# Performance work log

Hardware: AMD Instinct MI355X
Metric: run time of the kernel (lower is better)

The kernel has to match this reference:

```python
import jax, jax.numpy as jnp
import numpy as np

EMBED_DIM = 768
NUM_HEADS = 12
HEAD_DIM = EMBED_DIM // NUM_HEADS
MEMORY_SIZE = 64
B, T = 8, 1024


def setup_inputs() -> dict:
    key = jax.random.key(0)
    ks = jax.random.split(key, 8)
    s = 0.02
    return {
        "x": jax.random.normal(ks[0], (B, T, EMBED_DIM), dtype=jnp.float32),
        "w_qkv": jax.random.normal(ks[1], (EMBED_DIM, 3 * EMBED_DIM), dtype=jnp.float32) * s,
        "b_qkv": jax.random.normal(ks[2], (3 * EMBED_DIM,), dtype=jnp.float32) * s,
        "w_out": jax.random.normal(ks[3], (EMBED_DIM, EMBED_DIM), dtype=jnp.float32) * s,
        "b_out": jax.random.normal(ks[4], (EMBED_DIM,), dtype=jnp.float32) * s,
        "w_mem": jax.random.normal(ks[5], (EMBED_DIM, EMBED_DIM), dtype=jnp.float32) * s,
        "b_mem": jax.random.normal(ks[6], (EMBED_DIM,), dtype=jnp.float32) * s,
        "memory": jax.random.normal(ks[7], (1, MEMORY_SIZE, EMBED_DIM), dtype=jnp.float32),
    }


def reference(x, w_qkv, b_qkv, w_out, b_out, w_mem, b_mem, memory):
    Bx, Tx, C = x.shape
    H, D = NUM_HEADS, HEAD_DIM
    scale = 1.0 / np.sqrt(D).astype(np.float32)

    # qkv projection -> (3, B, H, T, D)
    qkv = (x @ w_qkv + b_qkv).reshape(Bx, Tx, 3, H, D)
    qkv = jnp.transpose(qkv, (2, 0, 3, 1, 4))
    q, k, v = qkv[0], qkv[1], qkv[2]

    # full (non-causal) local attention over T
    scores = jnp.einsum("bhqd,bhkd->bhqk", q, k) * scale  # (B,H,T,T)
    local_out = jnp.einsum("bhqk,bhkd->bhqd", jax.nn.softmax(scores, axis=-1), v)

    # memory attention: projected memory serves as both K and V
    mem = memory @ w_mem + b_mem                      # (1, M, C)
    mem = jnp.broadcast_to(mem, (Bx, MEMORY_SIZE, C))
    mem_kv = jnp.transpose(mem.reshape(Bx, MEMORY_SIZE, H, D), (0, 2, 1, 3))  # (B,H,M,D)
    mem_scores = jnp.einsum("bhqd,bhmd->bhqm", q, mem_kv) * scale
    mem_out = jnp.einsum("bhqm,bhmd->bhqd", jax.nn.softmax(mem_scores, axis=-1), mem_kv)

    out = (local_out + mem_out).transpose(0, 2, 1, 3).reshape(Bx, Tx, C)
    return out @ w_out + b_out
```

## Files before the change

### kernel.cpp

```cpp
#include <hip/hip_runtime.h>

#define EMBED 768
#define NH 12
#define HD 64
#define MEMN 64
#define BB 8
#define TT 1024
#define ROWS 8192
#define QKV_N 2304
#define QSZ 6291456

typedef short bf16x8_t __attribute__((ext_vector_type(8)));
typedef float f32x4_t __attribute__((ext_vector_type(4)));

__device__ __forceinline__ unsigned short f2b(float f){
    union { float f; unsigned int i; } v; v.f = f;
    unsigned int x = v.i;
    unsigned int r = x + 0x7fffu + ((x >> 16) & 1u);
    return (unsigned short)(r >> 16);
}
__device__ __forceinline__ unsigned short f2b_ru(float f){
    union { float f; unsigned int i; } v; v.f = f;
    return (unsigned short)((v.i + 0x8000u) >> 16);
}

__device__ __forceinline__ void gl16(const unsigned short* g, unsigned short* l){
    __builtin_amdgcn_global_load_lds(
        (const __attribute__((address_space(1))) void*)g,
        (__attribute__((address_space(3))) void*)l,
        16, 0, 0);
}

#define PREP_CVT   3072
#define PREP_TQKV  4800
#define PREP_TOUT  5376
#define PREP_TOTAL 5388

__global__ __launch_bounds__(256) void prep_kernel(
    const float* __restrict__ x,
    const float* __restrict__ w_qkv,
    const float* __restrict__ w_out,
    const float* __restrict__ memory,
    const float* __restrict__ w_mem,
    const float* __restrict__ b_mem,
    unsigned short* __restrict__ xb,
    unsigned short* __restrict__ wqkvT,
    unsigned short* __restrict__ woutT,
    unsigned short* __restrict__ mem_k,
    unsigned short* __restrict__ mem_v)
{
    __shared__ unsigned short pool[5120];
    const int bid = blockIdx.x;
    const int t = threadIdx.x;

    if (bid < PREP_CVT) {
        int i = bid * 2048 + t * 8;
        float4 f0 = *(const float4*)&x[i];
        float4 f1 = *(const float4*)&x[i + 4];
        union { bf16x8_t v; unsigned short s[8]; } u;
        u.s[0] = f2b(f0.x); u.s[1] = f2b(f0.y); u.s[2] = f2b(f0.z); u.s[3] = f2b(f0.w);
        u.s[4] = f2b(f1.x); u.s[5] = f2b(f1.y); u.s[6] = f2b(f1.z); u.s[7] = f2b(f1.w);
        *(bf16x8_t*)&xb[i] = u.v;
    } else if (bid < PREP_TOUT) {
        const float* in; unsigned short* out; int R, C, loc;
        if (bid < PREP_TQKV) { in = w_qkv; out = wqkvT; R = EMBED; C = QKV_N; loc = bid - PREP_CVT; }
        else                 { in = w_out; out = woutT; R = EMBED; C = EMBED; loc = bid - PREP_TQKV; }
        int nbc = C / 32;
        int bc = (loc % nbc) * 32, br = (loc / nbc) * 32;
        unsigned short (*tile)[33] = (unsigned short(*)[33])pool;
        int lr = t >> 5, lc = t & 31;
        for (int i = 0; i < 4; i++) {
            int r = lr + i * 8;
            tile[r][lc] = f2b(in[(size_t)(br + r) * C + bc + lc]);
        }
        __syncthreads();
        for (int i = 0; i < 4; i++) {
            int r = lr + i * 8;
            out[(size_t)(bc + r) * R + br + lc] = tile[lc][r];
        }
    } else {
        unsigned short (*As)[40] = (unsigned short(*)[40])pool;
        unsigned short (*Bs)[40] = (unsigned short(*)[40])(pool + 2560);
        int wave = t >> 6, lane = t & 63;
        int ln = lane & 15, lq = lane >> 4;
        int bn = (bid - PREP_TOUT) * 64;
        const int K = EMBED, N = EMBED;

        f32x4_t acc[4];
        for (int i = 0; i < 4; i++) acc[i] = (f32x4_t)(0.f);
        int sm = t >> 2, sk = (t & 3) * 8;
        int bk = t >> 3, bn8 = (t & 7) * 8;

        for (int k0 = 0; k0 < K; k0 += 32) {
            __syncthreads();
            {
                float4 f0 = *(const float4*)&memory[(size_t)sm * K + k0 + sk];
                float4 f1 = *(const float4*)&memory[(size_t)sm * K + k0 + sk + 4];
                unsigned short* ap = &As[sm][sk];
                ap[0] = f2b(f0.x); ap[1] = f2b(f0.y); ap[2] = f2b(f0.z); ap[3] = f2b(f0.w);
                ap[4] = f2b(f1.x); ap[5] = f2b(f1.y); ap[6] = f2b(f1.z); ap[7] = f2b(f1.w);
            }
            {
                float4 g0 = *(const float4*)&w_mem[(size_t)(k0 + bk) * N + bn + bn8];
                float4 g1 = *(const float4*)&w_mem[(size_t)(k0 + bk) * N + bn + bn8 + 4];
                Bs[bn8 + 0][bk] = f2b(g0.x); Bs[bn8 + 1][bk] = f2b(g0.y);
                Bs[bn8 + 2][bk] = f2b(g0.z); Bs[bn8 + 3][bk] = f2b(g0.w);
                Bs[bn8 + 4][bk] = f2b(g1.x); Bs[bn8 + 5][bk] = f2b(g1.y);
                Bs[bn8 + 6][bk] = f2b(g1.z); Bs[bn8 + 7][bk] = f2b(g1.w);
            }
            __syncthreads();
            bf16x8_t a = *(bf16x8_t*)&As[wave * 16 + ln][lq * 8];
            for (int nt = 0; nt < 4; nt++) {
                bf16x8_t bf = *(bf16x8_t*)&Bs[nt * 16 + ln][lq * 8];
                acc[nt] = __builtin_amdgcn_mfma_f32_16x16x32_bf16(a, bf, acc[nt], 0, 0, 0);
            }
        }
        for (int nt = 0; nt < 4; nt++) {
            int c = bn + nt * 16 + ln;
            float bv = b_mem[c];
            for (int r = 0; r < 4; r++) {
                int row = wave * 16 + lq * 4 + r;
                int h = c >> 6, d = c & 63;
                unsigned short o = f2b(acc[nt][r] + bv);
                mem_k[((h * 64 + row) << 6) + d] = o;
                mem_v[((h * 64 + d) << 6) + row] = o;
            }
        }
    }
}

__global__ __launch_bounds__(256) void vtrans_kernel(
    const unsigned short* __restrict__ in, unsigned short* __restrict__ out)
{
    __shared__ unsigned short tile[64][72];
    int t0 = blockIdx.x * 64;
    int bh = blockIdx.y;
    const unsigned short* ip = in + ((size_t)bh * TT + t0) * 64;
    unsigned short* op = out + ((size_t)bh * 64) * TT + t0;
    int t = threadIdx.x;
    for (int i = 0; i < 2; i++) {
        int idx = i * 256 + t;
        int r = idx >> 3, c8 = (idx & 7) * 8;
        *(bf16x8_t*)&tile[r][c8] = *(const bf16x8_t*)&ip[(size_t)r * 64 + c8];
    }
    __syncthreads();
    for (int i = 0; i < 2; i++) {
        int idx = i * 256 + t;
        int d = idx >> 3, tc8 = (idx & 7) * 8;
        union { bf16x8_t v; unsigned short s[8]; } u;
        for (int j = 0; j < 8; j++) u.s[j] = tile[tc8 + j][d];
        *(bf16x8_t*)&op[(size_t)d * TT + tc8] = u.v;
    }
}

__global__ __launch_bounds__(512) void gemm512(
    const unsigned short* __restrict__ A,
    const unsigned short* __restrict__ BT,
    const float* __restrict__ bias,
    unsigned short* __restrict__ dq,
    unsigned short* __restrict__ dkv,
    int M, int N, int K)
{
    __shared__ unsigned short As[16384];
    __shared__ unsigned short Bs[8192];
    const int t = threadIdx.x;
    const int wave = t >> 6, lane = t & 63;
    const int ln = lane & 15, lq = lane >> 4;
    const int wm = (wave >> 1) * 64, wn = (wave & 1) * 64;
    const int bm = blockIdx.y * 256, bn = blockIdx.x * 128;

    f32x4_t acc[4][4];
    for (int i = 0; i < 4; i++)
        for (int j = 0; j < 4; j++) acc[i][j] = (f32x4_t)(0.f);

    const int rl8 = lane >> 3;
    const int swz = ((lane & 7) ^ rl8) * 8;
    const unsigned short* Ap = A + (size_t)(bm + wave * 32 + rl8) * K + swz;
    const unsigned short* Bp = BT + (size_t)(bn + wave * 16 + rl8) * K + swz;
    unsigned short* asd = &As[wave * 2048];
    unsigned short* bsd = &Bs[wave * 1024];

    const int e0 = (lq ^ (ln & 7)) * 8;
    const int e1 = e0 ^ 32;

    for (int k0 = 0; k0 < K; k0 += 64) {
        __syncthreads();
        for (int i = 0; i < 4; i++)
            gl16(Ap + (size_t)(i * 8) * K + k0, asd + i * 512);
        for (int i = 0; i < 2; i++)
            gl16(Bp + (size_t)(i * 8) * K + k0, bsd + i * 512);
        __syncthreads();

        {
            bf16x8_t af[4], bfr[4];
            for (int mt = 0; mt < 4; mt++)
                af[mt] = *(bf16x8_t*)&As[(wm + mt * 16 + ln) * 64 + e0];
            for (int nt = 0; nt < 4; nt++)
                bfr[nt] = *(bf16x8_t*)&Bs[(wn + nt * 16 + ln) * 64 + e0];
            for (int mt = 0; mt < 4; mt++)
                for (int nt = 0; nt < 4; nt++)
                    acc[mt][nt] = __builtin_amdgcn_mfma_f32_16x16x32_bf16(
                        af[mt], bfr[nt], acc[mt][nt], 0, 0, 0);
        }
        {
            bf16x8_t af[4], bfr[4];
            for (int mt = 0; mt < 4; mt++)
                af[mt] = *(bf16x8_t*)&As[(wm + mt * 16 + ln) * 64 + e1];
            for (int nt = 0; nt < 4; nt++)
                bfr[nt] = *(bf16x8_t*)&Bs[(wn + nt * 16 + ln) * 64 + e1];
            for (int mt = 0; mt < 4; mt++)
                for (int nt = 0; nt < 4; nt++)
                    acc[mt][nt] = __builtin_amdgcn_mfma_f32_16x16x32_bf16(
                        af[mt], bfr[nt], acc[mt][nt], 0, 0, 0);
        }
    }

    const float QSCALE = 0.125f * 1.44269504088896340736f;
    const int s = bn / 768;
    for (int nt = 0; nt < 4; nt++) {
        int c = bn + wn + nt * 16 + ln;
        int rem = c - s * 768;
        int h = rem >> 6, d = rem & 63;
        float bv = bias[c];
        for (int mt = 0; mt < 4; mt++) {
            for (int r = 0; r < 4; r++) {
                int row = bm + wm + mt * 16 + lq * 4 + r;
                float val = acc[mt][nt][r] + bv;
                if (s == 0) {
                    dq[(size_t)row * 768 + rem] = f2b(val * QSCALE);
                } else {
                    int bb = row >> 10, tt = row & 1023;
                    dkv[(size_t)(s - 1) * QSZ +
                        (((size_t)(bb * 12 + h) * 1024 + tt) << 6) + d] = f2b(val);
                }
            }
        }
    }
}

__global__ __launch_bounds__(256) void gemm_bt(
    const unsigned short* __restrict__ A,
    const unsigned short* __restrict__ BT,
    const float* __restrict__ bias,
    float* __restrict__ df,
    int M, int N, int K)
{
    __shared__ unsigned short As[8192];
    __shared__ unsigned short Bs[8192];
    const int t = threadIdx.x;
    const int wave = t >> 6, lane = t & 63;
    const int ln = lane & 15, lq = lane >> 4;
    const int wm = (wave >> 1) * 64, wn = (wave & 1) * 64;
    const int bm = blockIdx.y * 128, bn = blockIdx.x * 128;

    f32x4_t acc[4][4];
    for (int i = 0; i < 4; i++)
        for (int j = 0; j < 4; j++) acc[i][j] = (f32x4_t)(0.f);

    const int rl8 = lane >> 3;
    const int swz = ((lane & 7) ^ rl8) * 8;
    const unsigned short* Ap = A + (size_t)(bm + wave * 32 + rl8) * K + swz;
    const unsigned short* Bp = BT + (size_t)(bn + wave * 32 + rl8) * K + swz;
    unsigned short* asd = &As[wave * 2048];
    unsigned short* bsd = &Bs[wave * 2048];

    const int e0 = (lq ^ (ln & 7)) * 8;
    const int e1 = e0 ^ 32;

    for (int k0 = 0; k0 < K; k0 += 64) {
        __syncthreads();
        for (int i = 0; i < 4; i++) {
            gl16(Ap + (size_t)(i * 8) * K + k0, asd + i * 512);
            gl16(Bp + (size_t)(i * 8) * K + k0, bsd + i * 512);
        }
        __syncthreads();

        {
            bf16x8_t af[4], bfr[4];
            for (int mt = 0; mt < 4; mt++)
                af[mt] = *(bf16x8_t*)&As[(wm + mt * 16 + ln) * 64 + e0];
            for (int nt = 0; nt < 4; nt++)
                bfr[nt] = *(bf16x8_t*)&Bs[(wn + nt * 16 + ln) * 64 + e0];
            for (int mt = 0; mt < 4; mt++)
                for (int nt = 0; nt < 4; nt++)
                    acc[mt][nt] = __builtin_amdgcn_mfma_f32_16x16x32_bf16(
                        af[mt], bfr[nt], acc[mt][nt], 0, 0, 0);
        }
        {
            bf16x8_t af[4], bfr[4];
            for (int mt = 0; mt < 4; mt++)
                af[mt] = *(bf16x8_t*)&As[(wm + mt * 16 + ln) * 64 + e1];
            for (int nt = 0; nt < 4; nt++)
                bfr[nt] = *(bf16x8_t*)&Bs[(wn + nt * 16 + ln) * 64 + e1];
            for (int mt = 0; mt < 4; mt++)
                for (int nt = 0; nt < 4; nt++)
                    acc[mt][nt] = __builtin_amdgcn_mfma_f32_16x16x32_bf16(
                        af[mt], bfr[nt], acc[mt][nt], 0, 0, 0);
        }
    }

    for (int nt = 0; nt < 4; nt++) {
        int c = bn + wn + nt * 16 + ln;
        float bv = bias[c];
        for (int mt = 0; mt < 4; mt++)
            for (int r = 0; r < 4; r++) {
                int row = bm + wm + mt * 16 + lq * 4 + r;
                df[(size_t)row * N + c] = acc[mt][nt][r] + bv;
            }
    }
}

__global__ __launch_bounds__(512) void attn_kernel(
    unsigned short* __restrict__ qio,
    const unsigned short* __restrict__ k_ws,
    const unsigned short* __restrict__ vT_ws,
    const unsigned short* __restrict__ mem_k,
    const unsigned short* __restrict__ mem_v)
{
    __shared__ unsigned short Qs[8192];
    __shared__ unsigned short Ks[8192];
    __shared__ unsigned short Vs[8192];
    unsigned short* Ps = Qs;

    const int t = threadIdx.x;
    const int wave = t >> 6, lane = t & 63;
    const int ln = lane & 15, lq = lane >> 4;
    const int rl = lane >> 3;
    const int cl = ((lane & 7) ^ rl) * 8;

    int bid = blockIdx.x;
    int xcd = bid & 7, rest = bid >> 3;
    int bh = xcd * 12 + (rest >> 3);
    int qt = rest & 7;
    int b = bh / 12, h = bh - b * 12;

    unsigned short* qp = qio + ((size_t)(b * TT + qt * 128)) * 768 + h * 64;
    const unsigned short* kp = k_ws + (size_t)bh * TT * 64;
    const unsigned short* vp = vT_ws + ((size_t)bh << 16);
    const unsigned short* mkp = mem_k + h * 4096;
    const unsigned short* mvp = mem_v + h * 4096;

    {
        const unsigned short* qg = qp + (size_t)(wave * 16 + rl) * 768 + cl;
        gl16(qg, &Qs[wave * 1024]);
        gl16(qg + (size_t)8 * 768, &Qs[wave * 1024 + 512]);
    }
    __syncthreads();
    const int e0 = (lq ^ (ln & 7)) * 8;
    const int e1 = ((lq ^ (ln & 7)) ^ 4) * 8;
    bf16x8_t aq0 = *(bf16x8_t*)&Qs[(wave * 16 + ln) * 64 + e0];
    bf16x8_t aq1 = *(bf16x8_t*)&Qs[(wave * 16 + ln) * 64 + e1];

    const unsigned short* kg = kp + (wave * 16 + rl) * 64 + cl;
    const unsigned short* vg = vp + (size_t)((wave & 3) * 16 + rl) * 1024 + (wave >> 2) * 64 + cl;

    const int hi3 = ln >> 3, lo3 = ln & 7;
    const int pm = (lq & 1) << 2;
    const int pw0 = (wave * 16 + lq * 4) * 64 + lo3;

    float lsum[4] = {0.f, 0.f, 0.f, 0.f};
    f32x4_t accO[4];
    for (int nt = 0; nt < 4; nt++) accO[nt] = (f32x4_t)(0.f);

    for (int kt = 0; kt < 8; kt++) {
        __syncthreads();
        gl16(kg + kt * 8192,        &Ks[wave * 1024]);
        gl16(kg + kt * 8192 + 512,  &Ks[wave * 1024 + 512]);
        gl16(vg + kt * 128,                 &Vs[wave * 1024]);
        gl16(vg + (size_t)8 * 1024 + kt * 128, &Vs[wave * 1024 + 512]);
        __syncthreads();

        for (int half = 0; half < 2; half++) {
            const unsigned short* Kh = &Ks[half * 4096];
            const unsigned short* Vh = &Vs[half * 4096];
            f32x4_t s[4];
            for (int nt = 0; nt < 4; nt++) s[nt] = (f32x4_t)(0.f);
            for (int nt = 0; nt < 4; nt++)
                s[nt] = __builtin_amdgcn_mfma_f32_16x16x32_bf16(
                    aq0, *(bf16x8_t*)&Kh[(nt * 16 + ln) * 64 + e0], s[nt], 0, 0, 0);
            for (int nt = 0; nt < 4; nt++)
                s[nt] = __builtin_amdgcn_mfma_f32_16x16x32_bf16(
                    aq1, *(bf16x8_t*)&Kh[(nt * 16 + ln) * 64 + e1], s[nt], 0, 0, 0);

            for (int nt = 0; nt < 4; nt++) {
                for (int r = 0; r < 4; r++) {
                    float p = __builtin_amdgcn_exp2f(s[nt][r]);
                    lsum[r] += p;
                    int chp = (nt * 2 + hi3) ^ pm ^ r;
                    Ps[pw0 + r * 64 + chp * 8] = f2b_ru(p);
                }
            }
            bf16x8_t a0 = *(bf16x8_t*)&Ps[(wave * 16 + ln) * 64 + e0];
            bf16x8_t a1 = *(bf16x8_t*)&Ps[(wave * 16 + ln) * 64 + e1];
            for (int nt = 0; nt < 4; nt++) {
                accO[nt] = __builtin_amdgcn_mfma_f32_16x16x32_bf16(
                    a0, *(bf16x8_t*)&Vh[(nt * 16 + ln) * 64 + e0], accO[nt], 0, 0, 0);
                accO[nt] = __builtin_amdgcn_mfma_f32_16x16x32_bf16(
                    a1, *(bf16x8_t*)&Vh[(nt * 16 + ln) * 64 + e1], accO[nt], 0, 0, 0);
            }
        }
    }

    __syncthreads();
    gl16(mkp + (wave * 8 + rl) * 64 + cl, &Ks[wave * 512]);
    gl16(mvp + (wave * 8 + rl) * 64 + cl, &Vs[wave * 512]);
    __syncthreads();

    f32x4_t s2[4];
    for (int nt = 0; nt < 4; nt++) s2[nt] = (f32x4_t)(0.f);
    for (int nt = 0; nt < 4; nt++)
        s2[nt] = __builtin_amdgcn_mfma_f32_16x16x32_bf16(
            aq0, *(bf16x8_t*)&Ks[(nt * 16 + ln) * 64 + e0], s2[nt], 0, 0, 0);
    for (int nt = 0; nt < 4; nt++)
        s2[nt] = __builtin_amdgcn_mfma_f32_16x16x32_bf16(
            aq1, *(bf16x8_t*)&Ks[(nt * 16 + ln) * 64 + e1], s2[nt], 0, 0, 0);

    float l2[4] = {0.f, 0.f, 0.f, 0.f};
    for (int nt = 0; nt < 4; nt++) {
        for (int r = 0; r < 4; r++) {
            float p = __builtin_amdgcn_exp2f(s2[nt][r]);
            l2[r] += p;
            int chp = (nt * 2 + hi3) ^ pm ^ r;
            Ps[pw0 + r * 64 + chp * 8] = f2b_ru(p);
        }
    }
    f32x4_t accM[4];
    for (int nt = 0; nt < 4; nt++) accM[nt] = (f32x4_t)(0.f);
    {
        bf16x8_t a0 = *(bf16x8_t*)&Ps[(wave * 16 + ln) * 64 + e0];
        bf16x8_t a1 = *(bf16x8_t*)&Ps[(wave * 16 + ln) * 64 + e1];
        for (int nt = 0; nt < 4; nt++) {
            accM[nt] = __builtin_amdgcn_mfma_f32_16x16x32_bf16(
                a0, *(bf16x8_t*)&Vs[(nt * 16 + ln) * 64 + e0], accM[nt], 0, 0, 0);
            accM[nt] = __builtin_amdgcn_mfma_f32_16x16x32_bf16(
                a1, *(bf16x8_t*)&Vs[(nt * 16 + ln) * 64 + e1], accM[nt], 0, 0, 0);
        }
    }

    float inv[4], inv2[4];
    for (int r = 0; r < 4; r++) {
        float a = lsum[r], c = l2[r];
        a += __shfl_xor(a, 1); a += __shfl_xor(a, 2);
        a += __shfl_xor(a, 4); a += __shfl_xor(a, 8);
        c += __shfl_xor(c, 1); c += __shfl_xor(c, 2);
        c += __shfl_xor(c, 4); c += __shfl_xor(c, 8);
        inv[r] = 1.f / a;
        inv2[r] = 1.f / c;
    }

    for (int nt = 0; nt < 4; nt++) {
        for (int r = 0; r < 4; r++) {
            int lrow = wave * 16 + lq * 4 + r;
            int lcol = nt * 16 + ln;
            float val = accO[nt][r] * inv[r] + accM[nt][r] * inv2[r];
            qp[(size_t)lrow * 768 + lcol] = f2b(val);
        }
    }
}

extern "C" void kernel_launch(void* const* d_in, const int* in_sizes, int n_in,
                              void* d_out, int out_size, void* d_ws, size_t ws_size,
                              hipStream_t stream) {
    const float* x      = (const float*)d_in[0];
    const float* w_qkv  = (const float*)d_in[1];
    const float* b_qkv  = (const float*)d_in[2];
    const float* w_out  = (const float*)d_in[3];
    const float* b_out  = (const float*)d_in[4];
    const float* w_mem  = (const float*)d_in[5];
    const float* b_mem  = (const float*)d_in[6];
    const float* memory = (const float*)d_in[7];

    unsigned short* ws = (unsigned short*)d_ws;
    unsigned short* q_ws   = ws;
    unsigned short* k_ws   = ws + (size_t)QSZ;
    unsigned short* woutT  = ws + 3 * (size_t)QSZ;
    unsigned short* mem_k  = woutT + (size_t)EMBED * EMBED;
    unsigned short* mem_v  = mem_k + (size_t)NH * MEMN * HD;

    unsigned short* xb    = (unsigned short*)d_out;
    unsigned short* wqkvT = xb + (size_t)QSZ;
    unsigned short* vT    = (unsigned short*)d_out;

    prep_kernel<<<PREP_TOTAL, 256, 0, stream>>>(
        x, w_qkv, w_out, memory, w_mem, b_mem, xb, wqkvT, woutT, mem_k, mem_v);

    gemm512<<<dim3(QKV_N / 128, ROWS / 256), 512, 0, stream>>>(
        xb, wqkvT, b_qkv, q_ws, k_ws, ROWS, QKV_N, EMBED);

    vtrans_kernel<<<dim3(TT / 64, BB * NH), 256, 0, stream>>>(k_ws + (size_t)QSZ, vT);

    attn_kernel<<<8 * NH * BB, 512, 0, stream>>>(q_ws, k_ws, vT, mem_k, mem_v);

    gemm_bt<<<dim3(EMBED / 128, ROWS / 128), 256, 0, stream>>>(
        q_ws, woutT, b_out, (float*)d_out, ROWS, EMBED, EMBED);
}
```

Measured before the change: 245.0 us.

## Double-buffer LDS in QKV and output GEMMs with block remap and MFMA priority

Both GEMM kernels now keep two LDS buffers, so the global-to-LDS loads for the next K tile are issued before computing on the current tile, removing one barrier per iteration. All LDS fragment reads are hoisted ahead of the MFMA chain, and s_setprio raises wave priority around the MFMAs. The QKV GEMM also remaps block IDs in a strided, XCD-aware order to change which tiles run together. The cost is doubled LDS use (96KB for gemm512), which may lower occupancy, and the hardcoded remap constants (72, 18) only fit the 18x32 grid.

```diff
diff --git a/kernel.cpp b/kernel.cpp
--- a/kernel.cpp
+++ b/kernel.cpp
@@ -161,13 +161,17 @@
     unsigned short* __restrict__ dkv,
     int M, int N, int K)
 {
-    __shared__ unsigned short As[16384];
-    __shared__ unsigned short Bs[8192];
+    __shared__ unsigned short As[2][16384];
+    __shared__ unsigned short Bs[2][8192];
     const int t = threadIdx.x;
     const int wave = t >> 6, lane = t & 63;
     const int ln = lane & 15, lq = lane >> 4;
     const int wm = (wave >> 1) * 64, wn = (wave & 1) * 64;
-    const int bm = blockIdx.y * 256, bn = blockIdx.x * 128;
+
+    int bid0 = blockIdx.y * gridDim.x + blockIdx.x;
+    int bid = (bid0 & 7) * 72 + (bid0 >> 3);
+    int by = bid / 18, bx = bid - by * 18;
+    const int bm = by * 256, bn = bx * 128;
 
     f32x4_t acc[4][4];
     for (int i = 0; i < 4; i++)
@@ -177,43 +181,56 @@
     const int swz = ((lane & 7) ^ rl8) * 8;
     const unsigned short* Ap = A + (size_t)(bm + wave * 32 + rl8) * K + swz;
     const unsigned short* Bp = BT + (size_t)(bn + wave * 16 + rl8) * K + swz;
-    unsigned short* asd = &As[wave * 2048];
-    unsigned short* bsd = &Bs[wave * 1024];
 
     const int e0 = (lq ^ (ln & 7)) * 8;
     const int e1 = e0 ^ 32;
 
-    for (int k0 = 0; k0 < K; k0 += 64) {
+    auto compute = [&](const unsigned short* Ac, const unsigned short* Bc) {
+        bf16x8_t af0[4], af1[4], bf0[4], bf1[4];
+#pragma unroll
+        for (int mt = 0; mt < 4; mt++) {
+            af0[mt] = *(const bf16x8_t*)&Ac[(wm + mt * 16 + ln) * 64 + e0];
+            af1[mt] = *(const bf16x8_t*)&Ac[(wm + mt * 16 + ln) * 64 + e1];
+        }
+#pragma unroll
+        for (int nt = 0; nt < 4; nt++) {
+            bf0[nt] = *(const bf16x8_t*)&Bc[(wn + nt * 16 + ln) * 64 + e0];
+            bf1[nt] = *(const bf16x8_t*)&Bc[(wn + nt * 16 + ln) * 64 + e1];
+        }
+        __builtin_amdgcn_s_setprio(1);
+#pragma unroll
+        for (int mt = 0; mt < 4; mt++)
+#pragma unroll
+            for (int nt = 0; nt < 4; nt++)
+                acc[mt][nt] = __builtin_amdgcn_mfma_f32_16x16x32_bf16(
+                    af0[mt], bf0[nt], acc[mt][nt], 0, 0, 0);
+#pragma unroll
+        for (int mt = 0; mt < 4; mt++)
+#pragma unroll
+            for (int nt = 0; nt < 4; nt++)
+                acc[mt][nt] = __builtin_amdgcn_mfma_f32_16x16x32_bf16(
+                    af1[mt], bf1[nt], acc[mt][nt], 0, 0, 0);
+        __builtin_amdgcn_s_setprio(0);
+    };
+
+    for (int i = 0; i < 4; i++)
+        gl16(Ap + (size_t)(i * 8) * K, &As[0][wave * 2048 + i * 512]);
+    for (int i = 0; i < 2; i++)
+        gl16(Bp + (size_t)(i * 8) * K, &Bs[0][wave * 1024 + i * 512]);
+    __syncthreads();
+
+    int cur = 0;
+    for (int k0 = 0; k0 < K - 64; k0 += 64) {
+        const int nb = cur ^ 1;
+        for (int i = 0; i < 4; i++)
+            gl16(Ap + (size_t)(i * 8) * K + k0 + 64, &As[nb][wave * 2048 + i * 512]);
+        for (int i = 0; i < 2; i++)
+            gl16(Bp + (size_t)(i * 8) * K + k0 + 64, &Bs[nb][wave * 1024 + i * 512]);
+        compute(As[cur], Bs[cur]);
         __syncthreads();
-        for (int i = 0; i < 4; i++)
-            gl16(Ap + (size_t)(i * 8) * K + k0, asd + i * 512);
-        for (int i = 0; i < 2; i++)
-            gl16(Bp + (size_t)(i * 8) * K + k0, bsd + i * 512);
-        __syncthreads();
-
-        {
-            bf16x8_t af[4], bfr[4];
-            for (int mt = 0; mt < 4; mt++)
-                af[mt] = *(bf16x8_t*)&As[(wm + mt * 16 + ln) * 64 + e0];
-            for (int nt = 0; nt < 4; nt++)
-                bfr[nt] = *(bf16x8_t*)&Bs[(wn + nt * 16 + ln) * 64 + e0];
-            for (int mt = 0; mt < 4; mt++)
-                for (int nt = 0; nt < 4; nt++)
-                    acc[mt][nt] = __builtin_amdgcn_mfma_f32_16x16x32_bf16(
-                        af[mt], bfr[nt], acc[mt][nt], 0, 0, 0);
-        }
-        {
-            bf16x8_t af[4], bfr[4];
-            for (int mt = 0; mt < 4; mt++)
-                af[mt] = *(bf16x8_t*)&As[(wm + mt * 16 + ln) * 64 + e1];
-            for (int nt = 0; nt < 4; nt++)
-                bfr[nt] = *(bf16x8_t*)&Bs[(wn + nt * 16 + ln) * 64 + e1];
-            for (int mt = 0; mt < 4; mt++)
-                for (int nt = 0; nt < 4; nt++)
-                    acc[mt][nt] = __builtin_amdgcn_mfma_f32_16x16x32_bf16(
-                        af[mt], bfr[nt], acc[mt][nt], 0, 0, 0);
-        }
-    }
+        cur = nb;
+    }
+    compute(As[cur], Bs[cur]);
 
     const float QSCALE = 0.125f * 1.44269504088896340736f;
     const int s = bn / 768;
@@ -245,8 +262,8 @@
     float* __restrict__ df,
     int M, int N, int K)
 {
-    __shared__ unsigned short As[8192];
-    __shared__ unsigned short Bs[8192];
+    __shared__ unsigned short As[2][8192];
+    __shared__ unsigned short Bs[2][8192];
     const int t = threadIdx.x;
     const int wave = t >> 6, lane = t & 63;
     const int ln = lane & 15, lq = lane >> 4;
@@ -261,43 +278,56 @@
     const int swz = ((lane & 7) ^ rl8) * 8;
     const unsigned short* Ap = A + (size_t)(bm + wave * 32 + rl8) * K + swz;
     const unsigned short* Bp = BT + (size_t)(bn + wave * 32 + rl8) * K + swz;
-    unsigned short* asd = &As[wave * 2048];
-    unsigned short* bsd = &Bs[wave * 2048];
 
     const int e0 = (lq ^ (ln & 7)) * 8;
     const int e1 = e0 ^ 32;
 
-    for (int k0 = 0; k0 < K; k0 += 64) {
+    auto compute = [&](const unsigned short* Ac, const unsigned short* Bc) {
+        bf16x8_t af0[4], af1[4], bf0[4], bf1[4];
+#pragma unroll
+        for (int mt = 0; mt < 4; mt++) {
+            af0[mt] = *(const bf16x8_t*)&Ac[(wm + mt * 16 + ln) * 64 + e0];
+            af1[mt] = *(const bf16x8_t*)&Ac[(wm + mt * 16 + ln) * 64 + e1];
+        }
+#pragma unroll
+        for (int nt = 0; nt < 4; nt++) {
+            bf0[nt] = *(const bf16x8_t*)&Bc[(wn + nt * 16 + ln) * 64 + e0];
+            bf1[nt] = *(const bf16x8_t*)&Bc[(wn + nt * 16 + ln) * 64 + e1];
+        }
+        __builtin_amdgcn_s_setprio(1);
+#pragma unroll
+        for (int mt = 0; mt < 4; mt++)
+#pragma unroll
+            for (int nt = 0; nt < 4; nt++)
+                acc[mt][nt] = __builtin_amdgcn_mfma_f32_16x16x32_bf16(
+                    af0[mt], bf0[nt], acc[mt][nt], 0, 0, 0);
+#pragma unroll
+        for (int mt = 0; mt < 4; mt++)
+#pragma unroll
+            for (int nt = 0; nt < 4; nt++)
+                acc[mt][nt] = __builtin_amdgcn_mfma_f32_16x16x32_bf16(
+                    af1[mt], bf1[nt], acc[mt][nt], 0, 0, 0);
+        __builtin_amdgcn_s_setprio(0);
+    };
+
+    for (int i = 0; i < 4; i++) {
+        gl16(Ap + (size_t)(i * 8) * K, &As[0][wave * 2048 + i * 512]);
+        gl16(Bp + (size_t)(i * 8) * K, &Bs[0][wave * 2048 + i * 512]);
+    }
+    __syncthreads();
+
+    int cur = 0;
+    for (int k0 = 0; k0 < K - 64; k0 += 64) {
+        const int nb = cur ^ 1;
+        for (int i = 0; i < 4; i++) {
+            gl16(Ap + (size_t)(i * 8) * K + k0 + 64, &As[nb][wave * 2048 + i * 512]);
+            gl16(Bp + (size_t)(i * 8) * K + k0 + 64, &Bs[nb][wave * 2048 + i * 512]);
+        }
+        compute(As[cur], Bs[cur]);
         __syncthreads();
-        for (int i = 0; i < 4; i++) {
-            gl16(Ap + (size_t)(i * 8) * K + k0, asd + i * 512);
-            gl16(Bp + (size_t)(i * 8) * K + k0, bsd + i * 512);
-        }
-        __syncthreads();
-
-        {
-            bf16x8_t af[4], bfr[4];
-            for (int mt = 0; mt < 4; mt++)
-                af[mt] = *(bf16x8_t*)&As[(wm + mt * 16 + ln) * 64 + e0];
-            for (int nt = 0; nt < 4; nt++)
-                bfr[nt] = *(bf16x8_t*)&Bs[(wn + nt * 16 + ln) * 64 + e0];
-            for (int mt = 0; mt < 4; mt++)
-                for (int nt = 0; nt < 4; nt++)
-                    acc[mt][nt] = __builtin_amdgcn_mfma_f32_16x16x32_bf16(
-                        af[mt], bfr[nt], acc[mt][nt], 0, 0, 0);
-        }
-        {
-            bf16x8_t af[4], bfr[4];
-            for (int mt = 0; mt < 4; mt++)
-                af[mt] = *(bf16x8_t*)&As[(wm + mt * 16 + ln) * 64 + e1];
-            for (int nt = 0; nt < 4; nt++)
-                bfr[nt] = *(bf16x8_t*)&Bs[(wn + nt * 16 + ln) * 64 + e1];
-            for (int mt = 0; mt < 4; mt++)
-                for (int nt = 0; nt < 4; nt++)
-                    acc[mt][nt] = __builtin_amdgcn_mfma_f32_16x16x32_bf16(
-                        af[mt], bfr[nt], acc[mt][nt], 0, 0, 0);
-        }
-    }
+        cur = nb;
+    }
+    compute(As[cur], Bs[cur]);
 
     for (int nt = 0; nt < 4; nt++) {
         int c = bn + wn + nt * 16 + ln;
```

Result: slower. 251.1 us (+2.5%).
